# Kernel tuning notes

Hardware: AMD Instinct MI355X
Metric: run time of the kernel (lower is better)

Reference implementation:

```python
import jax, jax.numpy as jnp
import numpy as np

B, T, OBS, H, L, C, A = 64, 128, 512, 1024, 32, 32, 18
LC = L * C
ALPHA, FREE_NATS = 0.8, 1.0


def setup_inputs() -> dict:
    key = jax.random.key(0)
    ks = jax.random.split(key, 16)
    w = lambda k, s: jax.random.normal(k, s, dtype=jnp.float32) * 0.02
    z = lambda s: jnp.zeros(s, jnp.float32)
    return {
        "obs_seq": jax.random.normal(ks[0], (B, T, OBS), dtype=jnp.float32),
        "gumbel": jax.random.gumbel(ks[1], (T, B, L, C), dtype=jnp.float32),
        "enc_w1": w(ks[2], (OBS, H)), "enc_b1": z((H,)),
        "enc_w2": w(ks[3], (H, H)), "enc_b2": z((H,)),
        "gru_wih": w(ks[4], (3 * H, LC + A)), "gru_whh": w(ks[5], (3 * H, H)),
        "gru_bih": z((3 * H,)), "gru_bhh": z((3 * H,)),
        "prior_w": w(ks[6], (H, LC)), "prior_b": z((LC,)),
        "post_w": w(ks[7], (2 * H, LC)), "post_b": z((LC,)),
        "dec_w1": w(ks[8], (H + LC, H)), "dec_b1": z((H,)),
        "dec_w2": w(ks[9], (H, OBS)), "dec_b2": z((OBS,)),
        "rew_w": w(ks[10], (H + LC, 1)), "rew_b": z((1,)),
        "act_seq": jax.random.randint(ks[11], (B, T), 0, A),
    }


def _gumbel_hard(logits, g):
    # gumbel-softmax (tau=1) with straight-through hard sample
    y = jax.nn.softmax(logits + g, axis=-1)              # [B, L, C]
    y_hard = jax.nn.one_hot(jnp.argmax(y, -1), C, dtype=y.dtype)
    return jax.lax.stop_gradient(y_hard - y) + y


def reference(obs_seq, gumbel, enc_w1, enc_b1, enc_w2, enc_b2,
              gru_wih, gru_whh, gru_bih, gru_bhh,
              prior_w, prior_b, post_w, post_b,
              dec_w1, dec_b1, dec_w2, dec_b2, rew_w, rew_b, act_seq):
    # MLP encoder over flattened (B*T) observations
    e = jax.nn.relu(obs_seq.reshape(-1, OBS) @ enc_w1 + enc_b1)
    e = jax.nn.relu(e @ enc_w2 + enc_b2).reshape(B, T, H)

    act_oh = jax.nn.one_hot(act_seq, A, dtype=jnp.float32)  # [B, T, A]

    def gru_cell(h, x):  # torch nn.GRU gate order: r, z, n
        gi = x @ gru_wih.T + gru_bih
        gh = h @ gru_whh.T + gru_bhh
        ir, iz, inn = jnp.split(gi, 3, axis=-1)
        hr, hz, hn = jnp.split(gh, 3, axis=-1)
        r = jax.nn.sigmoid(ir + hr)
        zg = jax.nn.sigmoid(iz + hz)
        n = jnp.tanh(inn + r * hn)
        return (1.0 - zg) * n + zg * h

    h0 = jnp.zeros((B, H), jnp.float32)
    logits0 = (jnp.concatenate([h0, e[:, 0]], -1) @ post_w + post_b).reshape(B, L, C)
    samp0 = _gumbel_hard(logits0, gumbel[0]).reshape(B, LC)

    def step(carry, xs):
        h, samp = carry
        a_t, e_next, g = xs
        h_new = gru_cell(h, jnp.concatenate([samp, a_t], -1))
        logits = (jnp.concatenate([h_new, e_next], -1) @ post_w + post_b).reshape(B, L, C)
        samp_new = _gumbel_hard(logits, g).reshape(B, LC)
        # emit hidden state and the sample that was fed to the GRU (samples[:-1])
        return (h_new, samp_new), (h_new, samp)

    xs = (jnp.transpose(act_oh[:, :T - 1], (1, 0, 2)),
          jnp.transpose(e[:, 1:], (1, 0, 2)),
          gumbel[1:])
    _, (hs, samples) = jax.lax.scan(step, (h0, samp0), xs)
    hs = jnp.transpose(hs, (1, 0, 2))          # [B, T-1, H]
    samples = jnp.transpose(samples, (1, 0, 2))  # [B, T-1, LC]

    prior_logits = (hs @ prior_w + prior_b).reshape(B, T - 1, L, C)
    post_logits = (jnp.concatenate([hs, e[:, 1:]], -1) @ post_w + post_b).reshape(B, T - 1, L, C)

    lp = jax.nn.log_softmax(prior_logits, -1)
    lq = jax.nn.log_softmax(post_logits, -1)
    kl_f = (jnp.exp(lq) * (lq - lp)).sum(-1).sum(-1)  # KL(post||prior), sum latents
    kl_r = (jnp.exp(lp) * (lp - lq)).sum(-1).sum(-1)
    kl_loss = jnp.maximum(ALPHA * kl_f + (1.0 - ALPHA) * kl_r, FREE_NATS).mean()

    di = jnp.concatenate([hs, samples], -1)  # [B, T-1, H+LC]
    recon = jax.nn.relu(di @ dec_w1 + dec_b1) @ dec_w2 + dec_b2  # [B, T-1, OBS]
    pred_reward = (di @ rew_w + rew_b)[..., 0]  # [B, T-1]

    return recon, pred_reward, kl_loss, hs, samples
```

## Files before the change

kernel.cpp:

```cpp
#include <hip/hip_runtime.h>
#include <hip/hip_bf16.h>
#include <math.h>

#define BB 64
#define TT 128
#define T1 127
#define OBS 512
#define HH 1024
#define LL 32
#define CC 32
#define AA 18
#define KIN 1042
#define G3 3072
#define NWG 256

__device__ __forceinline__ float4 ld4(const float* p) { return *(const float4*)p; }

__global__ __launch_bounds__(256) void tr_k(const float* __restrict__ wih, float* __restrict__ wihT)
{
    __shared__ float tile[32][33];
    int g0 = blockIdx.x * 32;
    int k0 = blockIdx.y * 32;
    int tx = threadIdx.x, ty = threadIdx.y;
    #pragma unroll
    for (int r = 0; r < 32; r += 8) {
        int g = g0 + ty + r, k = k0 + tx;
        tile[ty + r][tx] = (k < KIN) ? wih[(size_t)g * KIN + k] : 0.f;
    }
    __syncthreads();
    #pragma unroll
    for (int r = 0; r < 32; r += 8) {
        int k = k0 + ty + r, g = g0 + tx;
        if (k < KIN) wihT[(size_t)k * G3 + g] = tile[tx][ty + r];
    }
}

__global__ __launch_bounds__(256) void tr2_k(const float* __restrict__ src, float* __restrict__ dst)
{
    __shared__ float tile[32][33];
    int r0 = blockIdx.x * 32;
    int c0 = blockIdx.y * 32;
    int tx = threadIdx.x, ty = threadIdx.y;
    #pragma unroll
    for (int rr = 0; rr < 32; rr += 8)
        tile[ty + rr][tx] = src[(size_t)(r0 + ty + rr) * HH + c0 + tx];
    __syncthreads();
    #pragma unroll
    for (int rr = 0; rr < 32; rr += 8)
        dst[(size_t)(c0 + ty + rr) * HH + r0 + tx] = tile[tx][ty + rr];
}

template<int RELU, int HAS_EXTRA, int AAL>
__global__ __launch_bounds__(256) void gemm_k(const float* __restrict__ A, const float* __restrict__ Bm,
    float* __restrict__ Cm, int M, int N, int K,
    const float* __restrict__ bias, const float* __restrict__ extra)
{
    __shared__ float As[16][132];
    __shared__ float Bs[16][132];
    int tid = threadIdx.x;
    int tx = tid & 15, ty = tid >> 4;
    int m0 = blockIdx.y * 128, n0 = blockIdx.x * 128;
    float acc[8][8];
    #pragma unroll
    for (int i = 0; i < 8; ++i)
        #pragma unroll
        for (int j = 0; j < 8; ++j) acc[i][j] = 0.f;

    int arow = tid >> 1;
    int ak0  = (tid & 1) * 8;
    int am   = m0 + arow;

    float  ar[8];
    float4 br[2];

    auto loadA = [&](int kt) {
        if (am < M) {
            const float* ap = A + (size_t)am * K + kt + ak0;
            if (AAL) {
                float4 v0 = ld4(ap), v1 = ld4(ap + 4);
                ar[0] = v0.x; ar[1] = v0.y; ar[2] = v0.z; ar[3] = v0.w;
                ar[4] = v1.x; ar[5] = v1.y; ar[6] = v1.z; ar[7] = v1.w;
            } else {
                #pragma unroll
                for (int e = 0; e < 8; ++e) ar[e] = ap[e];
            }
        } else {
            #pragma unroll
            for (int e = 0; e < 8; ++e) ar[e] = 0.f;
        }
    };
    auto loadB = [&](int kt) {
        #pragma unroll
        for (int i2 = 0; i2 < 2; ++i2) {
            int idx = tid * 2 + i2;
            int kk = idx >> 5, c4 = idx & 31;
            br[i2] = ld4(Bm + (size_t)(kt + kk) * N + n0 + c4 * 4);
        }
    };

    loadA(0); loadB(0);

    for (int kt = 0; kt < K; kt += 16) {
        #pragma unroll
        for (int e = 0; e < 8; ++e) As[ak0 + e][arow] = ar[e];
        #pragma unroll
        for (int i2 = 0; i2 < 2; ++i2) {
            int idx = tid * 2 + i2;
            int kk = idx >> 5, c4 = idx & 31;
            *(float4*)&Bs[kk][c4 * 4] = br[i2];
        }
        __syncthreads();
        if (kt + 16 < K) { loadA(kt + 16); loadB(kt + 16); }
        #pragma unroll
        for (int k = 0; k < 16; ++k) {
            float av[8], bv[8];
            *(float4*)&av[0] = *(const float4*)&As[k][ty * 8];
            *(float4*)&av[4] = *(const float4*)&As[k][ty * 8 + 4];
            *(float4*)&bv[0] = *(const float4*)&Bs[k][tx * 8];
            *(float4*)&bv[4] = *(const float4*)&Bs[k][tx * 8 + 4];
            #pragma unroll
            for (int i = 0; i < 8; ++i)
                #pragma unroll
                for (int j = 0; j < 8; ++j)
                    acc[i][j] = fmaf(av[i], bv[j], acc[i][j]);
        }
        __syncthreads();
    }
    #pragma unroll
    for (int i = 0; i < 8; ++i) {
        int m = m0 + ty * 8 + i;
        if (m >= M) break;
        #pragma unroll
        for (int jh = 0; jh < 2; ++jh) {
            int n = n0 + tx * 8 + jh * 4;
            float4 v;
            v.x = acc[i][jh * 4 + 0] + bias[n + 0];
            v.y = acc[i][jh * 4 + 1] + bias[n + 1];
            v.z = acc[i][jh * 4 + 2] + bias[n + 2];
            v.w = acc[i][jh * 4 + 3] + bias[n + 3];
            if (HAS_EXTRA) {
                float4 e = ld4(extra + (size_t)m * N + n);
                v.x += e.x; v.y += e.y; v.z += e.z; v.w += e.w;
            }
            if (RELU) {
                v.x = fmaxf(v.x, 0.f); v.y = fmaxf(v.y, 0.f);
                v.z = fmaxf(v.z, 0.f); v.w = fmaxf(v.w, 0.f);
            }
            *(float4*)(Cm + (size_t)m * N + n) = v;
        }
    }
}

__global__ __launch_bounds__(256) void samp0_k(const float* __restrict__ epost, const float* __restrict__ gumbel,
                                               float* __restrict__ samples_out, int* __restrict__ sidx)
{
    int b = blockIdx.x;
    int tid = threadIdx.x;
    int l = tid >> 3, s = tid & 7;
    const float* lg = epost + ((size_t)b * TT + 0) * HH + l * 32;
    const float* gm = gumbel + (((size_t)0 * BB + b) * LL + l) * CC;
    float u[4];
    #pragma unroll
    for (int i = 0; i < 4; ++i) { int c = s * 4 + i; u[i] = lg[c] + gm[c]; }
    float best = u[0]; int bi = s * 4;
    #pragma unroll
    for (int i = 1; i < 4; ++i) { if (u[i] > best) { best = u[i]; bi = s * 4 + i; } }
    for (int m = 1; m < 8; m <<= 1) {
        float ov = __shfl_xor(best, m, 8);
        int   oi = __shfl_xor(bi, m, 8);
        if (ov > best || (ov == best && oi < bi)) { best = ov; bi = oi; }
    }
    float* so = samples_out + ((size_t)b * T1 + 0) * HH + l * 32;
    #pragma unroll
    for (int i = 0; i < 4; ++i) { int c = s * 4 + i; so[c] = (c == bi) ? 1.f : 0.f; }
    if (s == 0) sidx[((size_t)0 * BB + b) * LL + l] = bi;
}

__device__ __forceinline__ void gbar(unsigned int* __restrict__ flags, int bi, int bid)
{
    __syncthreads();
    unsigned int* f = flags + (size_t)bi * NWG;
    int tid = threadIdx.x;
    if (tid < 64) {
        if (tid == 0)
            __hip_atomic_store(&f[bid], 1u, __ATOMIC_RELAXED, __HIP_MEMORY_SCOPE_AGENT);
        int it = 0;
        for (;;) {
            unsigned int v0 = __hip_atomic_load(&f[tid],       __ATOMIC_RELAXED, __HIP_MEMORY_SCOPE_AGENT);
            unsigned int v1 = __hip_atomic_load(&f[64 + tid],  __ATOMIC_RELAXED, __HIP_MEMORY_SCOPE_AGENT);
            unsigned int v2 = __hip_atomic_load(&f[128 + tid], __ATOMIC_RELAXED, __HIP_MEMORY_SCOPE_AGENT);
            unsigned int v3 = __hip_atomic_load(&f[192 + tid], __ATOMIC_RELAXED, __HIP_MEMORY_SCOPE_AGENT);
            if (__all((v0 & v1 & v2 & v3) != 0)) break;
            __builtin_amdgcn_s_sleep(4);
            if (((++it) & 2047) == 2047 && tid == 0) {
                __hip_atomic_store(&f[bid], 1u, __ATOMIC_RELEASE, __HIP_MEMORY_SCOPE_AGENT);
                (void)__hip_atomic_load(&f[bid], __ATOMIC_ACQUIRE, __HIP_MEMORY_SCOPE_AGENT);
            }
        }
    }
    __syncthreads();
}

__global__ __launch_bounds__(512) void scan_k(
    float* __restrict__ hseq, float* __restrict__ hso,
    const float* __restrict__ wihT, const float* __restrict__ whh,
    const float* __restrict__ bih, const float* __restrict__ bhh,
    int* __restrict__ sidx, const int* __restrict__ act,
    const float* __restrict__ postwT, const float* __restrict__ epost,
    const float* __restrict__ gum, float* __restrict__ plog,
    float* __restrict__ smo, unsigned int* __restrict__ flags)
{
    __shared__ __align__(16) char smraw[129664];
    float (*wfull)[12][516] = (float(*)[12][516])smraw;
    char* U = smraw + 49536;
    float (*h_s)[64][132] = (float(*)[64][132])U;
    int   (*off_s)[33]    = (int(*)[33])(U + 67584);
    float (*ps)[4]        = (float(*)[4])(U + 76032);
    float (*hb_s)[8][132]  = (float(*)[8][132])U;
    float (*wb_s)[32][132] = (float(*)[32][132])(U + 8448);
    float* psb             = (float*)(U + 42240);

    int tid = threadIdx.x;
    int kh = tid >> 8;
    int r  = tid & 255;
    int bid = blockIdx.x;
    int sb = (bid & 7) * 32 + (bid >> 3);
    int j0 = sb * 4;
    int ab = r >> 2, q = r & 3, j = j0 + q;
    int l  = bid & 31;
    int bc = bid >> 5;
    int b0 = bc * 8;
    int b8 = r >> 5;
    int c  = r & 31;
    int n0 = l * 32;

    for (int i = tid; i < 3072; i += 512) {
        int k4 = i & 127;
        int rowi = i >> 7;
        int kh2 = (rowi >= 12) ? 1 : 0;
        int rr = rowi - kh2 * 12;
        int g = (rr >> 2) * 1024 + j0 + (rr & 3);
        *(float4*)&wfull[kh2][rr][k4 * 4] = ld4(whh + (size_t)g * HH + kh2 * 512 + k4 * 4);
    }
    __syncthreads();

    const int kbase = kh * 512;

    for (int t = 1; t <= 127; ++t) {
        {
            const float* hprev = hseq + (size_t)(t - 1) * 65536;
            const int* sidx_prev = sidx + (size_t)(t - 1) * 2048;

            for (int i = tid; i < 64 * 33; i += 512) {
                int bb = i / 33, ll = i - bb * 33;
                off_s[bb][ll] = (ll < 32) ? (ll * 32 + sidx_prev[bb * 32 + ll])
                                          : (1024 + act[bb * TT + (t - 1)]);
            }
            __syncthreads();

            float a0 = 0.f, a1 = 0.f, a2 = 0.f, g2 = 0.f;
            if (kh == 0) {
                #pragma unroll
                for (int i = 0; i < 17; ++i) {
                    int o = off_s[ab][i];
                    const float* wp = wihT + (size_t)o * G3 + j;
                    a0 += wp[0]; a1 += wp[1024]; g2 += wp[2048];
                }
            } else {
                #pragma unroll
                for (int i = 17; i < 33; ++i) {
                    int o = off_s[ab][i];
                    const float* wp = wihT + (size_t)o * G3 + j;
                    a0 += wp[0]; a1 += wp[1024]; g2 += wp[2048];
                }
            }

            float4 hreg[8];
            auto loadH = [&](int kc) {
                #pragma unroll
                for (int m = 0; m < 8; ++m) {
                    int i = r + m * 256;
                    int row = i >> 5, c4 = i & 31;
                    hreg[m] = ld4(hprev + row * HH + kbase + kc * 128 + c4 * 4);
                }
            };
            loadH(0);
            for (int kc = 0; kc < 4; ++kc) {
                #pragma unroll
                for (int m = 0; m < 8; ++m) {
                    int i = r + m * 256;
                    int row = i >> 5, c4 = i & 31;
                    *(float4*)&h_s[kh][row][c4 * 4] = hreg[m];
                }
                __syncthreads();
                if (kc < 3) loadH(kc + 1);
                #pragma unroll 8
                for (int k4 = 0; k4 < 32; ++k4) {
                    float4 hv = *(const float4*)&h_s[kh][ab][k4 * 4];
                    float4 w0 = *(const float4*)&wfull[kh][q][kc * 128 + k4 * 4];
                    float4 w1 = *(const float4*)&wfull[kh][4 + q][kc * 128 + k4 * 4];
                    float4 w2 = *(const float4*)&wfull[kh][8 + q][kc * 128 + k4 * 4];
                    a0 += hv.x * w0.x + hv.y * w0.y + hv.z * w0.z + hv.w * w0.w;
                    a1 += hv.x * w1.x + hv.y * w1.y + hv.z * w1.z + hv.w * w1.w;
                    a2 += hv.x * w2.x + hv.y * w2.y + hv.z * w2.z + hv.w * w2.w;
                }
                __syncthreads();
            }
            if (kh == 1) { ps[r][0] = a0; ps[r][1] = a1; ps[r][2] = a2; ps[r][3] = g2; }
            __syncthreads();
            if (kh == 0) {
                float s0 = a0 + ps[r][0];
                float s1 = a1 + ps[r][1];
                float hn = a2 + ps[r][2] + bhh[2048 + j];
                float inn = g2 + ps[r][3] + bih[2048 + j];
                float rr = 1.f / (1.f + expf(-(s0 + bih[j] + bhh[j])));
                float zz = 1.f / (1.f + expf(-(s1 + bih[1024 + j] + bhh[1024 + j])));
                float nn = tanhf(inn + rr * hn);
                float hp = hprev[ab * HH + j];
                float hv = (1.f - zz) * nn + zz * hp;
                __hip_atomic_store(&hseq[(size_t)t * 65536 + ab * HH + j], hv,
                                   __ATOMIC_RELAXED, __HIP_MEMORY_SCOPE_AGENT);
                hso[((size_t)ab * T1 + (t - 1)) * HH + j] = hv;
            }
        }
        gbar(flags, (t - 1) * 2, bid);

        {
            const float* hcur = hseq + (size_t)t * 65536;
            float acc = 0.f;
            for (int kc = 0; kc < 4; ++kc) {
                int kb = kbase + kc * 128;
                {
                    int row = r >> 5, c4 = r & 31;
                    *(float4*)&hb_s[kh][row][c4 * 4] = ld4(hcur + (b0 + row) * HH + kb + c4 * 4);
                }
                #pragma unroll
                for (int ii = 0; ii < 4; ++ii) {
                    int slot = r + ii * 256;
                    int cc = slot >> 5, f4 = slot & 31;
                    *(float4*)&wb_s[kh][cc][f4 * 4] = ld4(postwT + (size_t)(n0 + cc) * HH + kb + f4 * 4);
                }
                __syncthreads();
                #pragma unroll 8
                for (int k4 = 0; k4 < 32; ++k4) {
                    float4 hv = *(const float4*)&hb_s[kh][b8][k4 * 4];
                    float4 wv = *(const float4*)&wb_s[kh][c][k4 * 4];
                    acc += hv.x * wv.x + hv.y * wv.y + hv.z * wv.z + hv.w * wv.w;
                }
                __syncthreads();
            }
            if (kh == 1) psb[r] = acc;
            __syncthreads();
            if (kh == 0) {
                int b = b0 + b8;
                int n = n0 + c;
                float lg = acc + psb[r] + epost[((size_t)b * TT + t) * HH + n];
                plog[((size_t)(t - 1) * BB + b) * HH + n] = lg;
                if (t <= 126) {
                    float u = lg + gum[(((size_t)t * BB + b) * LL + l) * CC + c];
                    float best = u; int bi = c;
                    for (int m = 1; m < 32; m <<= 1) {
                        float ov = __shfl_xor(best, m, 32);
                        int   oi = __shfl_xor(bi, m, 32);
                        if (ov > best || (ov == best && oi < bi)) { best = ov; bi = oi; }
                    }
                    smo[((size_t)b * T1 + t) * HH + n] = (c == bi) ? 1.f : 0.f;
                    if (c == 0)
                        __hip_atomic_store(&sidx[((size_t)t * BB + b) * LL + l], bi,
                                           __ATOMIC_RELAXED, __HIP_MEMORY_SCOPE_AGENT);
                }
            }
        }
        if (t < 127) gbar(flags, (t - 1) * 2 + 1, bid);
    }
}

__global__ __launch_bounds__(256) void kl_k(const float* __restrict__ prior,
    const float* __restrict__ plog, float* __restrict__ out)
{
    int rrow = blockIdx.x;
    int b = rrow / T1, i = rrow - b * T1;
    int tid = threadIdx.x;
    int l = tid >> 3, s = tid & 7;
    const float* pp = prior + (size_t)rrow * HH + l * 32;
    const float* qq = plog + ((size_t)i * BB + b) * HH + l * 32;
    float pv[4], qv[4];
    #pragma unroll
    for (int e = 0; e < 4; ++e) { int c = s * 4 + e; pv[e] = pp[c]; qv[e] = qq[c]; }
    float mp = fmaxf(fmaxf(pv[0], pv[1]), fmaxf(pv[2], pv[3]));
    float mq = fmaxf(fmaxf(qv[0], qv[1]), fmaxf(qv[2], qv[3]));
    for (int m = 1; m < 8; m <<= 1) {
        mp = fmaxf(mp, __shfl_xor(mp, m, 8));
        mq = fmaxf(mq, __shfl_xor(mq, m, 8));
    }
    float sp = 0.f, sq = 0.f;
    #pragma unroll
    for (int e = 0; e < 4; ++e) { sp += expf(pv[e] - mp); sq += expf(qv[e] - mq); }
    for (int m = 1; m < 8; m <<= 1) { sp += __shfl_xor(sp, m, 8); sq += __shfl_xor(sq, m, 8); }
    float lsp = mp + logf(sp), lsq = mq + logf(sq);
    float kf = 0.f, kr = 0.f;
    #pragma unroll
    for (int e = 0; e < 4; ++e) {
        float lp = pv[e] - lsp, lq = qv[e] - lsq;
        float eq = expf(lq), ep = expf(lp);
        kf += eq * (lq - lp); kr += ep * (lp - lq);
    }
    for (int m = 1; m < 8; m <<= 1) { kf += __shfl_xor(kf, m, 8); kr += __shfl_xor(kr, m, 8); }
    __shared__ float kfs[32], krs[32];
    if (s == 0) { kfs[l] = kf; krs[l] = kr; }
    __syncthreads();
    if (tid == 0) {
        float f = 0.f, r = 0.f;
        for (int l2 = 0; l2 < 32; ++l2) { f += kfs[l2]; r += krs[l2]; }
        float val = fmaxf(0.8f * f + 0.2f * r, 1.0f);
        atomicAdd(out, val * (1.0f / 8128.0f));
    }
}

__global__ __launch_bounds__(256) void gsum_k(const float* __restrict__ dw1bot,
    const int* __restrict__ sidx, float* __restrict__ gsum)
{
    int rrow = blockIdx.x;
    int b = rrow / T1, i = rrow - b * T1;
    __shared__ int offs[32];
    int tid = threadIdx.x;
    if (tid < 32) offs[tid] = tid * 32 + sidx[((size_t)i * BB + b) * LL + tid];
    __syncthreads();
    int n = tid * 4;
    float4 acc = make_float4(0.f, 0.f, 0.f, 0.f);
    #pragma unroll 4
    for (int l = 0; l < 32; ++l) {
        float4 v = ld4(dw1bot + (size_t)offs[l] * HH + n);
        acc.x += v.x; acc.y += v.y; acc.z += v.z; acc.w += v.w;
    }
    *(float4*)(gsum + (size_t)rrow * HH + n) = acc;
}

__global__ __launch_bounds__(256) void rew_k(const float* __restrict__ hs, const float* __restrict__ reww,
    const float* __restrict__ rewb, const int* __restrict__ sidx, float* __restrict__ pred)
{
    int rrow = blockIdx.x * 4 + (threadIdx.x >> 6);
    int lane = threadIdx.x & 63;
    int b = rrow / T1, i = rrow - b * T1;
    const float* hp = hs + (size_t)rrow * HH;
    float acc = 0.f;
    for (int k = lane; k < HH; k += 64) acc += hp[k] * reww[k];
    for (int m = 1; m < 64; m <<= 1) acc += __shfl_xor(acc, m, 64);
    if (lane == 0) {
        float g = 0.f;
        const int* sp = sidx + ((size_t)i * BB + b) * LL;
        for (int l = 0; l < 32; ++l) g += reww[1024 + l * 32 + sp[l]];
        pred[rrow] = acc + g + rewb[0];
    }
}

extern "C" void kernel_launch(void* const* d_in, const int* in_sizes, int n_in,
                              void* d_out, int out_size, void* d_ws, size_t ws_size,
                              hipStream_t stream) {
    const float* obs   = (const float*)d_in[0];
    const float* gum   = (const float*)d_in[1];
    const float* ew1   = (const float*)d_in[2];
    const float* eb1   = (const float*)d_in[3];
    const float* ew2   = (const float*)d_in[4];
    const float* eb2   = (const float*)d_in[5];
    const float* wih   = (const float*)d_in[6];
    const float* whh   = (const float*)d_in[7];
    const float* bih   = (const float*)d_in[8];
    const float* bhh   = (const float*)d_in[9];
    const float* priw  = (const float*)d_in[10];
    const float* prib  = (const float*)d_in[11];
    const float* postw = (const float*)d_in[12];
    const float* postb = (const float*)d_in[13];
    const float* dw1   = (const float*)d_in[14];
    const float* db1   = (const float*)d_in[15];
    const float* dw2   = (const float*)d_in[16];
    const float* db2   = (const float*)d_in[17];
    const float* reww  = (const float*)d_in[18];
    const float* rewb  = (const float*)d_in[19];
    const int*   act   = (const int*)d_in[20];
    (void)in_sizes; (void)n_in; (void)out_size; (void)ws_size;

    float* ws = (float*)d_ws;
    float* wihT   = ws;
    float* postwT = wihT + 3201024;
    float* bufA   = postwT + 1048576;
    float* bufB   = bufA + 8388608;
    float* plog   = bufB + 8388608;
    int*   sidx   = (int*)(plog + 8323072);
    unsigned int* flags = (unsigned int*)(sidx + 260096);

    float* out = (float*)d_out;
    float* recon = out;
    float* pred  = out + 4161536;
    float* klo   = pred + 8128;
    float* hso   = klo + 1;
    float* smo   = hso + 8323072;

    hipMemsetAsync(klo, 0, sizeof(float), stream);
    hipMemsetAsync(flags, 0, 253 * 256 * sizeof(unsigned int), stream);

    tr_k<<<dim3(96, 33), dim3(32, 8), 0, stream>>>(wih, wihT);
    tr2_k<<<dim3(32, 32), dim3(32, 8), 0, stream>>>(postw, postwT);
    gemm_k<1,0,1><<<dim3(8, 64), 256, 0, stream>>>(obs,  ew1, bufA, 8192, 1024, 512,  eb1, nullptr);
    gemm_k<1,0,1><<<dim3(8, 64), 256, 0, stream>>>(bufA, ew2, bufB, 8192, 1024, 1024, eb2, nullptr);
    gemm_k<0,0,1><<<dim3(8, 64), 256, 0, stream>>>(bufB, postw + 1024 * 1024, bufA, 8192, 1024, 1024, postb, nullptr);
    samp0_k<<<64, 256, 0, stream>>>(bufA, gum, smo, sidx);

    hipMemsetAsync(bufB, 0, 65536 * sizeof(float), stream);

    {
        float* hseq_p = bufB; float* hso_p = hso;
        const float* wihT_p = wihT; const float* whh_p = whh;
        const float* bih_p = bih; const float* bhh_p = bhh;
        int* sidx_p = sidx; const int* act_p = act;
        const float* postwT_p = postwT; const float* epost_p = bufA;
        const float* gum_p = gum; float* plog_p = plog; float* smo_p = smo;
        unsigned int* flags_p = flags;
        void* args[] = { &hseq_p, &hso_p, &wihT_p, &whh_p, &bih_p, &bhh_p,
                         &sidx_p, &act_p, &postwT_p, &epost_p, &gum_p, &plog_p, &smo_p, &flags_p };
        hipLaunchCooperativeKernel((const void*)scan_k, dim3(256), dim3(512), args, 0, stream);
    }

    gemm_k<0,0,0><<<dim3(8, 64), 256, 0, stream>>>(hso, priw, bufA, 8128, 1024, 1024, prib, nullptr);
    kl_k<<<8128, 256, 0, stream>>>(bufA, plog, klo);
    gsum_k<<<8128, 256, 0, stream>>>(dw1 + 1024 * 1024, sidx, plog);
    gemm_k<1,1,0><<<dim3(8, 64), 256, 0, stream>>>(hso, dw1, bufB, 8128, 1024, 1024, db1, plog);
    gemm_k<0,0,1><<<dim3(4, 64), 256, 0, stream>>>(bufB, dw2, recon, 8128, 512, 1024, db2, nullptr);
    rew_k<<<2032, 256, 0, stream>>>(hso, reww, rewb, sidx, pred);
}
```

Baseline: 6.422 ms.

## Split grid barrier and overlap recurrent matmul with sample barrier wait

The grid barrier is split into arrive and wait phases, so each block computes the h·Whh recurrent product before waiting for the previous step's sampled indices. The input-side gather (Wih rows selected by the one-hot samples) then runs after that wait. The recurrent and posterior matmuls are restructured: a k-split across 32 lanes with register-blocked accumulators over 8 batches × 2 columns × 3 gates, swizzled shared-memory layouts, and a shared-memory reduction. Shared memory use drops a lot, and posterior weights are read straight from global memory. The cost is extra reduction passes through shared memory and more register pressure.

```diff
diff --git a/kernel.cpp b/kernel.cpp
--- a/kernel.cpp
+++ b/kernel.cpp
@@ -15,6 +15,7 @@
 #define NWG 256
 
 __device__ __forceinline__ float4 ld4(const float* p) { return *(const float4*)p; }
+__device__ __forceinline__ float2 lds2(const float* p) { return *(const float2*)p; }
 
 __global__ __launch_bounds__(256) void tr_k(const float* __restrict__ wih, float* __restrict__ wihT)
 {
@@ -176,14 +177,16 @@
     if (s == 0) sidx[((size_t)0 * BB + b) * LL + l] = bi;
 }
 
-__device__ __forceinline__ void gbar(unsigned int* __restrict__ flags, int bi, int bid)
-{
-    __syncthreads();
-    unsigned int* f = flags + (size_t)bi * NWG;
+__device__ __forceinline__ void bar_arrive(unsigned int* __restrict__ f, int bid)
+{
+    __syncthreads();
+    if (threadIdx.x == 0)
+        __hip_atomic_store(&f[bid], 1u, __ATOMIC_RELAXED, __HIP_MEMORY_SCOPE_AGENT);
+}
+__device__ __forceinline__ void bar_wait(unsigned int* __restrict__ f, int bid)
+{
     int tid = threadIdx.x;
     if (tid < 64) {
-        if (tid == 0)
-            __hip_atomic_store(&f[bid], 1u, __ATOMIC_RELAXED, __HIP_MEMORY_SCOPE_AGENT);
         int it = 0;
         for (;;) {
             unsigned int v0 = __hip_atomic_load(&f[tid],       __ATOMIC_RELAXED, __HIP_MEMORY_SCOPE_AGENT);
@@ -201,6 +204,12 @@
     __syncthreads();
 }
 
+#define WF_BASE 0
+#define R1_BASE 13056
+#define R2_BASE 21760
+#define OFF_BASE 30208
+#define GATH_BASE 32320
+#define SM_TOT 33088
 __global__ __launch_bounds__(512) void scan_k(
     float* __restrict__ hseq, float* __restrict__ hso,
     const float* __restrict__ wihT, const float* __restrict__ whh,
@@ -210,168 +219,211 @@
     const float* __restrict__ gum, float* __restrict__ plog,
     float* __restrict__ smo, unsigned int* __restrict__ flags)
 {
-    __shared__ __align__(16) char smraw[129664];
-    float (*wfull)[12][516] = (float(*)[12][516])smraw;
-    char* U = smraw + 49536;
-    float (*h_s)[64][132] = (float(*)[64][132])U;
-    int   (*off_s)[33]    = (int(*)[33])(U + 67584);
-    float (*ps)[4]        = (float(*)[4])(U + 76032);
-    float (*hb_s)[8][132]  = (float(*)[8][132])U;
-    float (*wb_s)[32][132] = (float(*)[32][132])(U + 8448);
-    float* psb             = (float*)(U + 42240);
-
-    int tid = threadIdx.x;
-    int kh = tid >> 8;
-    int r  = tid & 255;
-    int bid = blockIdx.x;
-    int sb = (bid & 7) * 32 + (bid >> 3);
-    int j0 = sb * 4;
-    int ab = r >> 2, q = r & 3, j = j0 + q;
-    int l  = bid & 31;
-    int bc = bid >> 5;
-    int b0 = bc * 8;
-    int b8 = r >> 5;
-    int c  = r & 31;
-    int n0 = l * 32;
-
-    for (int i = tid; i < 3072; i += 512) {
-        int k4 = i & 127;
-        int rowi = i >> 7;
-        int kh2 = (rowi >= 12) ? 1 : 0;
-        int rr = rowi - kh2 * 12;
-        int g = (rr >> 2) * 1024 + j0 + (rr & 3);
-        *(float4*)&wfull[kh2][rr][k4 * 4] = ld4(whh + (size_t)g * HH + kh2 * 512 + k4 * 4);
-    }
-    __syncthreads();
-
-    const int kbase = kh * 512;
+    __shared__ float sm[SM_TOT];
+    int* off_s = (int*)&sm[OFF_BASE];
+
+    const int tid = threadIdx.x;
+    const int bid = blockIdx.x;
+    const int sb = (bid & 7) * 32 + (bid >> 3);
+    const int j0 = sb * 4;
+    const int bposA = tid >> 6;
+    const int cposA = (tid >> 5) & 1;
+    const int ksA   = tid & 31;
+    const int swzA  = ksA * 4 + 2 * (ksA >> 3);
+    const int l  = bid & 31;
+    const int bc = bid >> 5;
+    const int b0 = bc * 8;
+    const int cposB = tid >> 5;
+    const int ksB   = tid & 31;
+    const int n0 = l * 32;
+
+    for (int idx = tid; idx < 3072; idx += 512) {
+        int r = idx >> 8;
+        int rem = idx & 255;
+        int kc = rem >> 5, ks = rem & 31;
+        int g = r >> 2, q = r & 3;
+        float4 v = ld4(whh + (size_t)(g * 1024 + j0 + q) * HH + kc * 128 + ks * 4);
+        int ph = WF_BASE + r * 1088 + kc * 136 + ks * 4 + 2 * (ks >> 3) + ((r >> 1) & 1) * 2;
+        *(float2*)&sm[ph]     = make_float2(v.x, v.y);
+        *(float2*)&sm[ph + 2] = make_float2(v.z, v.w);
+    }
+    __syncthreads();
 
     for (int t = 1; t <= 127; ++t) {
+        const float* hprev = hseq + (size_t)(t - 1) * 65536;
+
+        float acc[2][3][8];
+        #pragma unroll
+        for (int jj = 0; jj < 2; ++jj)
+            #pragma unroll
+            for (int g = 0; g < 3; ++g)
+                #pragma unroll
+                for (int bb = 0; bb < 8; ++bb) acc[jj][g][bb] = 0.f;
+
+        const int rowbase = bposA * 8 + cposA * 4;
+        float4 pre[4];
+        #pragma unroll
+        for (int i = 0; i < 4; ++i)
+            pre[i] = ld4(hprev + (rowbase + i) * HH + ksA * 4);
+
+        for (int kc = 0; kc < 8; ++kc) {
+            __syncthreads();
+            #pragma unroll
+            for (int i = 0; i < 4; ++i) {
+                int row = rowbase + i;
+                int ph = R1_BASE + row * 136 + swzA + ((row >> 2) & 1) * 2;
+                *(float2*)&sm[ph]     = make_float2(pre[i].x, pre[i].y);
+                *(float2*)&sm[ph + 2] = make_float2(pre[i].z, pre[i].w);
+            }
+            __syncthreads();
+            if (kc < 7) {
+                #pragma unroll
+                for (int i = 0; i < 4; ++i)
+                    pre[i] = ld4(hprev + (rowbase + i) * HH + (kc + 1) * 128 + ksA * 4);
+            }
+            float2 h0[8], h1[8];
+            #pragma unroll
+            for (int bb = 0; bb < 8; ++bb) {
+                int row = bposA * 8 + bb;
+                int ph = R1_BASE + row * 136 + swzA + ((row >> 2) & 1) * 2;
+                h0[bb] = lds2(&sm[ph]); h1[bb] = lds2(&sm[ph + 2]);
+            }
+            #pragma unroll
+            for (int jj = 0; jj < 2; ++jj)
+                #pragma unroll
+                for (int g = 0; g < 3; ++g) {
+                    int r = g * 4 + cposA * 2 + jj;
+                    int ph = WF_BASE + r * 1088 + kc * 136 + swzA + ((r >> 1) & 1) * 2;
+                    float2 w0 = lds2(&sm[ph]), w1 = lds2(&sm[ph + 2]);
+                    #pragma unroll
+                    for (int bb = 0; bb < 8; ++bb)
+                        acc[jj][g][bb] += h0[bb].x * w0.x + h0[bb].y * w0.y
+                                        + h1[bb].x * w1.x + h1[bb].y * w1.y;
+                }
+        }
+
+        if (t > 1) bar_wait(flags + (size_t)(127 + t - 2) * NWG, bid);
+        #pragma unroll
+        for (int u = 0; u < 4; ++u) {
+            int i = tid + u * 512;
+            int b = i >> 5, l2 = i & 31;
+            off_s[b * 33 + l2] = l2 * 32 + sidx[(size_t)(t - 1) * 2048 + b * 32 + l2];
+        }
+        if (tid < 64) off_s[tid * 33 + 32] = 1024 + act[tid * TT + (t - 1)];
+        __syncthreads();
+
+        if (tid < 192) {
+            int g = tid >> 6, b = tid & 63;
+            float4 gv = make_float4(0.f, 0.f, 0.f, 0.f);
+            #pragma unroll 4
+            for (int i = 0; i < 33; ++i) {
+                int o = off_s[b * 33 + i];
+                float4 v = ld4(wihT + (size_t)o * G3 + g * 1024 + j0);
+                gv.x += v.x; gv.y += v.y; gv.z += v.z; gv.w += v.w;
+            }
+            *(float4*)&sm[GATH_BASE + (g * 64 + b) * 4] = gv;
+        }
+        int jo = 0, bo = 0; float hp = 0.f;
+        if (tid < 256) { jo = tid >> 6; bo = tid & 63; hp = hprev[bo * HH + j0 + jo]; }
+
+        float gsum0 = 0.f, gsum1 = 0.f, gsum2 = 0.f;
+        #pragma unroll
+        for (int g = 0; g < 3; ++g) {
+            __syncthreads();
+            #pragma unroll
+            for (int jj = 0; jj < 2; ++jj)
+                #pragma unroll
+                for (int bb = 0; bb < 8; ++bb)
+                    sm[R2_BASE + ((cposA * 2 + jj) * 64 + bposA * 8 + bb) * 33 + ksA] = acc[jj][g][bb];
+            __syncthreads();
+            if (tid < 256) {
+                float s = 0.f;
+                #pragma unroll
+                for (int k = 0; k < 32; ++k) s += sm[R2_BASE + (jo * 64 + bo) * 33 + k];
+                if (g == 0) gsum0 = s; else if (g == 1) gsum1 = s; else gsum2 = s;
+            }
+        }
+
+        if (tid < 256) {
+            int col = j0 + jo;
+            float gr = sm[GATH_BASE + (0 * 64 + bo) * 4 + jo];
+            float gz = sm[GATH_BASE + (1 * 64 + bo) * 4 + jo];
+            float gn = sm[GATH_BASE + (2 * 64 + bo) * 4 + jo];
+            float rr = 1.f / (1.f + expf(-(gr + bih[col] + gsum0 + bhh[col])));
+            float zz = 1.f / (1.f + expf(-(gz + bih[1024 + col] + gsum1 + bhh[1024 + col])));
+            float nn = tanhf(gn + bih[2048 + col] + rr * (gsum2 + bhh[2048 + col]));
+            float hv = (1.f - zz) * nn + zz * hp;
+            __hip_atomic_store(&hseq[(size_t)t * 65536 + bo * HH + col], hv,
+                               __ATOMIC_RELAXED, __HIP_MEMORY_SCOPE_AGENT);
+            hso[((size_t)bo * T1 + (t - 1)) * HH + col] = hv;
+        }
+        bar_arrive(flags + (size_t)(t - 1) * NWG, bid);
+        bar_wait(flags + (size_t)(t - 1) * NWG, bid);
+
+        const float* hcur = hseq + (size_t)t * 65536;
         {
-            const float* hprev = hseq + (size_t)(t - 1) * 65536;
-            const int* sidx_prev = sidx + (size_t)(t - 1) * 2048;
-
-            for (int i = tid; i < 64 * 33; i += 512) {
-                int bb = i / 33, ll = i - bb * 33;
-                off_s[bb][ll] = (ll < 32) ? (ll * 32 + sidx_prev[bb * 32 + ll])
-                                          : (1024 + act[bb * TT + (t - 1)]);
-            }
+            int b = cposB >> 1, ithalf = cposB & 1;
+            float4 v[4];
+            #pragma unroll
+            for (int e = 0; e < 4; ++e)
+                v[e] = ld4(hcur + (b0 + b) * HH + ksB * 32 + ithalf * 16 + e * 4);
             __syncthreads();
-
-            float a0 = 0.f, a1 = 0.f, a2 = 0.f, g2 = 0.f;
-            if (kh == 0) {
-                #pragma unroll
-                for (int i = 0; i < 17; ++i) {
-                    int o = off_s[ab][i];
-                    const float* wp = wihT + (size_t)o * G3 + j;
-                    a0 += wp[0]; a1 += wp[1024]; g2 += wp[2048];
+            #pragma unroll
+            for (int e = 0; e < 4; ++e) {
+                int it = ithalf * 4 + e;
+                int ph = R1_BASE + b * 1088 + ksB * 34 + it * 4 + ((it >> 2) & 1) * 2;
+                *(float2*)&sm[ph]     = make_float2(v[e].x, v[e].y);
+                *(float2*)&sm[ph + 2] = make_float2(v[e].z, v[e].w);
+            }
+            __syncthreads();
+        }
+        float accB[2][8];
+        #pragma unroll
+        for (int cc = 0; cc < 2; ++cc)
+            #pragma unroll
+            for (int b = 0; b < 8; ++b) accB[cc][b] = 0.f;
+        #pragma unroll
+        for (int it = 0; it < 8; ++it) {
+            float4 wv0 = ld4(postwT + (size_t)(n0 + cposB * 2 + 0) * HH + ksB * 32 + it * 4);
+            float4 wv1 = ld4(postwT + (size_t)(n0 + cposB * 2 + 1) * HH + ksB * 32 + it * 4);
+            #pragma unroll
+            for (int b = 0; b < 8; ++b) {
+                int ph = R1_BASE + b * 1088 + ksB * 34 + it * 4 + ((it >> 2) & 1) * 2;
+                float2 a0 = lds2(&sm[ph]), a1 = lds2(&sm[ph + 2]);
+                accB[0][b] += a0.x * wv0.x + a0.y * wv0.y + a1.x * wv0.z + a1.y * wv0.w;
+                accB[1][b] += a0.x * wv1.x + a0.y * wv1.y + a1.x * wv1.z + a1.y * wv1.w;
+            }
+        }
+        __syncthreads();
+        #pragma unroll
+        for (int cc = 0; cc < 2; ++cc)
+            #pragma unroll
+            for (int b = 0; b < 8; ++b)
+                sm[R2_BASE + (b * 32 + ksB) * 33 + cposB * 2 + cc] = accB[cc][b];
+        __syncthreads();
+        if (tid < 256) {
+            int b = tid >> 5, c = tid & 31;
+            float s = 0.f;
+            #pragma unroll
+            for (int k = 0; k < 32; ++k) s += sm[R2_BASE + (b * 32 + k) * 33 + c];
+            int bg = b0 + b, n = n0 + c;
+            float lg = s + epost[((size_t)bg * TT + t) * HH + n];
+            plog[((size_t)(t - 1) * BB + bg) * HH + n] = lg;
+            if (t <= 126) {
+                float u = lg + gum[(((size_t)t * BB + bg) * LL + l) * CC + c];
+                float best = u; int bi = c;
+                for (int m = 1; m < 32; m <<= 1) {
+                    float ov = __shfl_xor(best, m, 32);
+                    int   oi = __shfl_xor(bi, m, 32);
+                    if (ov > best || (ov == best && oi < bi)) { best = ov; bi = oi; }
                 }
-            } else {
-                #pragma unroll
-                for (int i = 17; i < 33; ++i) {
-                    int o = off_s[ab][i];
-                    const float* wp = wihT + (size_t)o * G3 + j;
-                    a0 += wp[0]; a1 += wp[1024]; g2 += wp[2048];
-                }
-            }
-
-            float4 hreg[8];
-            auto loadH = [&](int kc) {
-                #pragma unroll
-                for (int m = 0; m < 8; ++m) {
-                    int i = r + m * 256;
-                    int row = i >> 5, c4 = i & 31;
-                    hreg[m] = ld4(hprev + row * HH + kbase + kc * 128 + c4 * 4);
-                }
-            };
-            loadH(0);
-            for (int kc = 0; kc < 4; ++kc) {
-                #pragma unroll
-                for (int m = 0; m < 8; ++m) {
-                    int i = r + m * 256;
-                    int row = i >> 5, c4 = i & 31;
-                    *(float4*)&h_s[kh][row][c4 * 4] = hreg[m];
-                }
-                __syncthreads();
-                if (kc < 3) loadH(kc + 1);
-                #pragma unroll 8
-                for (int k4 = 0; k4 < 32; ++k4) {
-                    float4 hv = *(const float4*)&h_s[kh][ab][k4 * 4];
-                    float4 w0 = *(const float4*)&wfull[kh][q][kc * 128 + k4 * 4];
-                    float4 w1 = *(const float4*)&wfull[kh][4 + q][kc * 128 + k4 * 4];
-                    float4 w2 = *(const float4*)&wfull[kh][8 + q][kc * 128 + k4 * 4];
-                    a0 += hv.x * w0.x + hv.y * w0.y + hv.z * w0.z + hv.w * w0.w;
-                    a1 += hv.x * w1.x + hv.y * w1.y + hv.z * w1.z + hv.w * w1.w;
-                    a2 += hv.x * w2.x + hv.y * w2.y + hv.z * w2.z + hv.w * w2.w;
-                }
-                __syncthreads();
-            }
-            if (kh == 1) { ps[r][0] = a0; ps[r][1] = a1; ps[r][2] = a2; ps[r][3] = g2; }
-            __syncthreads();
-            if (kh == 0) {
-                float s0 = a0 + ps[r][0];
-                float s1 = a1 + ps[r][1];
-                float hn = a2 + ps[r][2] + bhh[2048 + j];
-                float inn = g2 + ps[r][3] + bih[2048 + j];
-                float rr = 1.f / (1.f + expf(-(s0 + bih[j] + bhh[j])));
-                float zz = 1.f / (1.f + expf(-(s1 + bih[1024 + j] + bhh[1024 + j])));
-                float nn = tanhf(inn + rr * hn);
-                float hp = hprev[ab * HH + j];
-                float hv = (1.f - zz) * nn + zz * hp;
-                __hip_atomic_store(&hseq[(size_t)t * 65536 + ab * HH + j], hv,
-                                   __ATOMIC_RELAXED, __HIP_MEMORY_SCOPE_AGENT);
-                hso[((size_t)ab * T1 + (t - 1)) * HH + j] = hv;
-            }
-        }
-        gbar(flags, (t - 1) * 2, bid);
-
-        {
-            const float* hcur = hseq + (size_t)t * 65536;
-            float acc = 0.f;
-            for (int kc = 0; kc < 4; ++kc) {
-                int kb = kbase + kc * 128;
-                {
-                    int row = r >> 5, c4 = r & 31;
-                    *(float4*)&hb_s[kh][row][c4 * 4] = ld4(hcur + (b0 + row) * HH + kb + c4 * 4);
-                }
-                #pragma unroll
-                for (int ii = 0; ii < 4; ++ii) {
-                    int slot = r + ii * 256;
-                    int cc = slot >> 5, f4 = slot & 31;
-                    *(float4*)&wb_s[kh][cc][f4 * 4] = ld4(postwT + (size_t)(n0 + cc) * HH + kb + f4 * 4);
-                }
-                __syncthreads();
-                #pragma unroll 8
-                for (int k4 = 0; k4 < 32; ++k4) {
-                    float4 hv = *(const float4*)&hb_s[kh][b8][k4 * 4];
-                    float4 wv = *(const float4*)&wb_s[kh][c][k4 * 4];
-                    acc += hv.x * wv.x + hv.y * wv.y + hv.z * wv.z + hv.w * wv.w;
-                }
-                __syncthreads();
-            }
-            if (kh == 1) psb[r] = acc;
-            __syncthreads();
-            if (kh == 0) {
-                int b = b0 + b8;
-                int n = n0 + c;
-                float lg = acc + psb[r] + epost[((size_t)b * TT + t) * HH + n];
-                plog[((size_t)(t - 1) * BB + b) * HH + n] = lg;
-                if (t <= 126) {
-                    float u = lg + gum[(((size_t)t * BB + b) * LL + l) * CC + c];
-                    float best = u; int bi = c;
-                    for (int m = 1; m < 32; m <<= 1) {
-                        float ov = __shfl_xor(best, m, 32);
-                        int   oi = __shfl_xor(bi, m, 32);
-                        if (ov > best || (ov == best && oi < bi)) { best = ov; bi = oi; }
-                    }
-                    smo[((size_t)b * T1 + t) * HH + n] = (c == bi) ? 1.f : 0.f;
-                    if (c == 0)
-                        __hip_atomic_store(&sidx[((size_t)t * BB + b) * LL + l], bi,
-                                           __ATOMIC_RELAXED, __HIP_MEMORY_SCOPE_AGENT);
-                }
-            }
-        }
-        if (t < 127) gbar(flags, (t - 1) * 2 + 1, bid);
+                smo[((size_t)bg * T1 + t) * HH + n] = (c == bi) ? 1.f : 0.f;
+                if (c == 0)
+                    __hip_atomic_store(&sidx[((size_t)t * BB + bg) * LL + l], bi,
+                                       __ATOMIC_RELAXED, __HIP_MEMORY_SCOPE_AGENT);
+            }
+        }
+        if (t <= 126) bar_arrive(flags + (size_t)(127 + t - 1) * NWG, bid);
     }
 }
 
```

After: 7.549 ms. 17.5% more time.
